# Kernel optimization log

Measured on AMD Instinct MI355X. Metric: run time of the kernel, lower is better.

Reference implementation:

```python
import jax, jax.numpy as jnp
import numpy as np

B, N, D_IN, D_OUT = 4, 2048, 1024, 1024


def setup_inputs() -> dict:
    key = jax.random.key(0)
    kx, kq, kk, kv = jax.random.split(key, 4)
    x = jax.random.normal(kx, (B, N, D_IN), dtype=jnp.float32)
    # torch Linear(d_in, d_out, bias=False): y = x @ W.T, W ~ U(-1/sqrt(d_in), 1/sqrt(d_in)).
    # Store as [d_in, d_out] so y = x @ W.
    bound = 1.0 / np.sqrt(D_IN)
    Wq = jax.random.uniform(kq, (D_IN, D_OUT), jnp.float32, -bound, bound)
    Wk = jax.random.uniform(kk, (D_IN, D_OUT), jnp.float32, -bound, bound)
    Wv = jax.random.uniform(kv, (D_IN, D_OUT), jnp.float32, -bound, bound)
    return {"x": x, "Wq": Wq, "Wk": Wk, "Wv": Wv}


def reference(x, Wq, Wk, Wv):
    # x: [B, N, d_in]
    q = jnp.einsum("bnd,de->bne", x, Wq)  # [B, N, d_out]
    k = jnp.einsum("bnd,de->bne", x, Wk)
    v = jnp.einsum("bnd,de->bne", x, Wv)
    n = x.shape[1]
    scores = jnp.einsum("bqe,bke->bqk", q, k)  # [B, N, N]
    causal = jnp.triu(jnp.ones((n, n), dtype=bool), k=1)  # True above diagonal -> masked
    scores = jnp.where(causal, -jnp.inf, scores)
    scale = 1.0 / jnp.sqrt(jnp.asarray(k.shape[-1], dtype=scores.dtype))
    weights = jax.nn.softmax(scores * scale, axis=-1)
    # dropout with drop_rate=0.0 is identity
    return jnp.einsum("bqk,bke->bqe", weights, v)  # [B, N, d_out]
```

## Files before the change

### kernel.cpp

```cpp
#include <hip/hip_runtime.h>

typedef float  f4v  __attribute__((ext_vector_type(4)));
typedef short  s8v  __attribute__((ext_vector_type(8)));

__device__ __forceinline__ ushort f2b(float f) {
    union { float f; unsigned int u; } v; v.f = f;
    unsigned int u = v.u;
    u += 0x7fffu + ((u >> 16) & 1u);
    return (ushort)(u >> 16);
}
__device__ __forceinline__ float b2f(ushort u) {
    union { unsigned int u; float f; } v; v.u = ((unsigned int)u) << 16;
    return v.f;
}

__device__ __forceinline__ void async16(const ushort* g, ushort* ldsp) {
    __builtin_amdgcn_global_load_lds(
        (const __attribute__((address_space(1))) unsigned int*)g,
        (__attribute__((address_space(3))) unsigned int*)ldsp, 16, 0, 0);
}

__global__ __launch_bounds__(256) void prep(const float* __restrict__ in,
                                            ushort* __restrict__ out,
                                            float* __restrict__ l,
                                            const float* __restrict__ w0,
                                            const float* __restrict__ w1,
                                            const float* __restrict__ w2,
                                            ushort* __restrict__ wt) {
    const int L = blockIdx.x, tid = threadIdx.x;
    if (L < 8192) {
        int i = L * 256 + tid;
        if (i < 8192) l[i] = 0.f;
        float4 f = ((const float4*)in)[i];
        ushort4 o;
        o.x = f2b(f.x); o.y = f2b(f.y); o.z = f2b(f.z); o.w = f2b(f.w);
        ((ushort4*)out)[i] = o;
        return;
    }
    __shared__ float tile[32][33];
    const int T = L - 8192;
    const int z = T >> 10, rem = T & 1023;
    const int bx = rem & 31, by = rem >> 5;
    const float* W = (z == 0) ? w0 : (z == 1 ? w1 : w2);
    ushort* O = wt + (size_t)z * (1024u * 1024u);
    int x0 = bx * 32, y0 = by * 32;
    int tx = tid & 31, ty = tid >> 5;
    for (int i = 0; i < 4; i++)
        tile[ty + i * 8][tx] = W[(size_t)(y0 + ty + i * 8) * 1024 + x0 + tx];
    __syncthreads();
    for (int i = 0; i < 4; i++)
        O[(size_t)(x0 + ty + i * 8) * 1024 + y0 + tx] = f2b(tile[tx][ty + i * 8]);
}


#define RD_A4(buf_)                                                                   \
    _Pragma("unroll") for (int mi = 0; mi < 4; mi++)                                  \
    _Pragma("unroll") for (int s = 0; s < 2; s++)                                     \
        af[mi][s] = *(const s8v*)&(buf_)[(wm + mi * 16 + l16) * 64 +                  \
                                         (((s * 4 + quad) ^ (l16 & 7)) * 8)];

#define RD_B2(buf_, NI0_)                                                             \
    _Pragma("unroll") for (int j = 0; j < 2; j++)                                     \
    _Pragma("unroll") for (int s = 0; s < 2; s++)                                     \
        bf[j][s] = *(const s8v*)&(buf_)[(wn + ((NI0_) + j) * 16 + l16) * 64 +         \
                                        (((s * 4 + quad) ^ (l16 & 7)) * 8)];

#define MFMA16(NI0_)                                                                  \
    _Pragma("unroll") for (int mi = 0; mi < 4; mi++)                                  \
    _Pragma("unroll") for (int j = 0; j < 2; j++)                                     \
    _Pragma("unroll") for (int s = 0; s < 2; s++)                                     \
        acc[mi][(NI0_) + j] = __builtin_amdgcn_mfma_f32_16x16x32_bf16(                \
            af[mi][s], bf[j][s], acc[mi][(NI0_) + j], 0, 0, 0);

#define RD_A4_TO(dst_, buf_)                                                          \
    _Pragma("unroll") for (int mi = 0; mi < 4; mi++)                                  \
    _Pragma("unroll") for (int s = 0; s < 2; s++)                                     \
        dst_[mi][s] = *(const s8v*)&(buf_)[(wm + mi * 16 + l16) * 64 +                \
                                           (((s * 4 + quad) ^ (l16 & 7)) * 8)];

#define RD_B2_TO(dst_, buf_, NI0_)                                                    \
    _Pragma("unroll") for (int j = 0; j < 2; j++)                                     \
    _Pragma("unroll") for (int s = 0; s < 2; s++)                                     \
        dst_[j][s] = *(const s8v*)&(buf_)[(wn + ((NI0_) + j) * 16 + l16) * 64 +       \
                                          (((s * 4 + quad) ^ (l16 & 7)) * 8)];

#define MFMA16F(af_, bf_, NI0_)                                                       \
    _Pragma("unroll") for (int mi = 0; mi < 4; mi++)                                  \
    _Pragma("unroll") for (int j = 0; j < 2; j++)                                     \
    _Pragma("unroll") for (int s = 0; s < 2; s++)                                     \
        acc[mi][(NI0_) + j] = __builtin_amdgcn_mfma_f32_16x16x32_bf16(                \
            af_[mi][s], bf_[j][s], acc[mi][(NI0_) + j], 0, 0, 0);

#define TILE3_NB(t_)                                                                  \
  {                                                                                   \
    const int kB = ((t_) + 1) * 64;                                                   \
    const int kA = ((t_) + 2) * 64;                                                   \
    s8v af[4][2], bf[2][2];                                                           \
    RD_A4(a0)                                                                         \
    RD_B2(b0, 0)                                                                      \
    if ((t_) < 15) {                                                                  \
        ISSUE_B(b1, kB, 0);                                                           \
        ISSUE_B(b1, kB, 1);                                                           \
        ISSUE_B(b1, kB, 2);                                                           \
    }                                                                                 \
    __builtin_amdgcn_s_setprio(1);                                                    \
    MFMA16(0)                                                                         \
    __builtin_amdgcn_s_setprio(0);                                                    \
    RD_B2(b0, 2)                                                                      \
    if ((t_) < 14) {                                                                  \
        ISSUE_A(a2, kA, 0);                                                           \
        ISSUE_A(a2, kA, 1);                                                           \
    }                                                                                 \
    __builtin_amdgcn_s_setprio(1);                                                    \
    MFMA16(2)                                                                         \
    __builtin_amdgcn_s_setprio(0);                                                    \
    RD_B2(b0, 4)                                                                      \
    if ((t_) < 14) {                                                                  \
        ISSUE_A(a2, kA, 2);                                                           \
        ISSUE_A(a2, kA, 3);                                                           \
    }                                                                                 \
    __builtin_amdgcn_s_setprio(1);                                                    \
    MFMA16(4)                                                                         \
    __builtin_amdgcn_s_setprio(0);                                                    \
    if ((t_) < 14)       asm volatile("s_waitcnt vmcnt(4)" ::: "memory");             \
    else if ((t_) == 14) asm volatile("s_waitcnt vmcnt(0)" ::: "memory");             \
    asm volatile("s_barrier" ::: "memory");                                           \
    ushort* ta = a0; a0 = a1; a1 = a2; a2 = ta;                                       \
    ushort* tb = b0; b0 = b1; b1 = tb;                                                \
  }

__global__ __launch_bounds__(512, 2) void gemm_qkv(const ushort* __restrict__ A,
                                                   const ushort* __restrict__ Wt,
                                                   ushort* __restrict__ q,
                                                   ushort* __restrict__ k,
                                                   ushort* __restrict__ vt) {
    constexpr int K = 1024;
    extern __shared__ ushort lds[];

    const int L = blockIdx.x;
    const int xcd = L & 7, idx = L >> 3;
    const int ci = xcd >> 1, cj = xcd & 1;
    const int mo = idx >> 3, no = idx & 7;
    const int m0 = (ci * 8 + mo) * 256;
    const int n0 = (cj * 8 + no) * 192;

    const int tid = threadIdx.x;
    const int w = tid >> 6, lane = tid & 63, quad = lane >> 4, l16 = lane & 15;
    const int wm = (w >> 1) * 64, wn = (w & 1) * 96;

    ushort* a0 = lds;
    ushort* a1 = lds + 16384;
    ushort* a2 = lds + 32768;
    ushort* b0 = lds + 49152;
    ushort* b1 = lds + 61440;

    const int lr = lane >> 3;
    const int lc8 = (lane & 7) ^ lr;
    const ushort* Ab = A  + (size_t)(m0 + w * 8 + lr) * K + lc8 * 8;
    const ushort* Bb = Wt + (size_t)(n0 + w * 8 + lr) * K + lc8 * 8;
    const int dW = w * 512;

#define ISSUE_A(buf_, kk_, a_) async16(Ab + (size_t)(a_) * 64 * K + (kk_), (buf_) + (a_) * 4096 + dW)
#define ISSUE_B(buf_, kk_, c_) async16(Bb + (size_t)(c_) * 64 * K + (kk_), (buf_) + (c_) * 4096 + dW)

    f4v acc[4][6];
    #pragma unroll
    for (int mi = 0; mi < 4; mi++)
        #pragma unroll
        for (int ni = 0; ni < 6; ni++) acc[mi][ni] = 0;

    #pragma unroll
    for (int a = 0; a < 4; a++) ISSUE_A(a0, 0, a);
    #pragma unroll
    for (int c = 0; c < 3; c++) ISSUE_B(b0, 0, c);
    #pragma unroll
    for (int a = 0; a < 4; a++) ISSUE_A(a1, 64, a);
    asm volatile("s_waitcnt vmcnt(4)" ::: "memory");
    asm volatile("s_barrier" ::: "memory");

    for (int t = 0; t < 16; ++t) TILE3_NB(t)

    #pragma unroll
    for (int mi = 0; mi < 4; mi++)
        #pragma unroll
        for (int ni = 0; ni < 6; ni++) {
            int row = m0 + wm + mi * 16 + quad * 4;
            int col = n0 + wn + ni * 16 + l16;
            int z = col >> 10, cz = col & 1023;
            f4v v = acc[mi][ni];
            if (z < 2) {
                ushort* C = (z == 0) ? q : k;
                #pragma unroll
                for (int rr = 0; rr < 4; rr++)
                    C[(size_t)(row + rr) * 1024 + cz] = f2b(v[rr]);
            } else {
                int b = row >> 11, tok = row & 2047;
                ushort4 pk;
                pk.x = f2b(v[0]); pk.y = f2b(v[1]); pk.z = f2b(v[2]); pk.w = f2b(v[3]);
                *(ushort4*)&vt[(size_t)b * (1024u * 2048u) + (size_t)cz * 2048 + tok] = pk;
            }
        }
#undef ISSUE_A
#undef ISSUE_B
}

__global__ __launch_bounds__(512, 2) void sgemm_qk(const ushort* __restrict__ Q,
                                                   const ushort* __restrict__ Km,
                                                   ushort* __restrict__ E,
                                                   float* __restrict__ l) {
    constexpr int K = 1024;
    extern __shared__ ushort lds[];

    const int L = blockIdx.x;
    const int xcd = L & 7, i = L >> 3;
    const int t = (xcd < 4) ? (xcd * 26 + i) : (104 + (xcd - 4) * 25 + i);
    const int b = t / 51;
    int tt = t - b * 51;
    int mt = 0;
    for (;; mt++) {
        int c = (4 * (mt + 1) + 2) / 3;
        if (tt < c) break;
        tt -= c;
    }
    const int nt = tt;
    const int m0 = mt * 256, n0 = nt * 192;
    const ushort* A  = Q  + (size_t)b * 2048 * 1024;
    const ushort* Bt = Km + (size_t)b * 2048 * 1024;
    ushort* Cb = E + (size_t)b * 2048 * 2048;
    float* lb = l + (size_t)b * 2048;

    const int tid = threadIdx.x;
    const int w = tid >> 6, lane = tid & 63, quad = lane >> 4, l16 = lane & 15;
    const int wm = (w >> 1) * 64, wn = (w & 1) * 96;

    ushort* a0 = lds;
    ushort* a1 = lds + 16384;
    ushort* a2 = lds + 32768;
    ushort* b0 = lds + 49152;
    ushort* b1 = lds + 61440;

    const int lr = lane >> 3;
    const int lc8 = (lane & 7) ^ lr;
    const ushort* Ab = A  + (size_t)(m0 + w * 8 + lr) * K + lc8 * 8;
    const ushort* Bb = Bt + (size_t)(n0 + w * 8 + lr) * K + lc8 * 8;
    const int dW = w * 512;

#define ISSUE_A(buf_, kk_, a_) async16(Ab + (size_t)(a_) * 64 * K + (kk_), (buf_) + (a_) * 4096 + dW)
#define ISSUE_B(buf_, kk_, c_) async16(Bb + (size_t)(c_) * 64 * K + (kk_), (buf_) + (c_) * 4096 + dW)

    f4v acc[4][6];
    #pragma unroll
    for (int mi = 0; mi < 4; mi++)
        #pragma unroll
        for (int ni = 0; ni < 6; ni++) acc[mi][ni] = 0;

    #pragma unroll
    for (int a = 0; a < 4; a++) ISSUE_A(a0, 0, a);
    #pragma unroll
    for (int c = 0; c < 3; c++) ISSUE_B(b0, 0, c);
    #pragma unroll
    for (int a = 0; a < 4; a++) ISSUE_A(a1, 64, a);
    asm volatile("s_waitcnt vmcnt(4)" ::: "memory");
    asm volatile("s_barrier" ::: "memory");

    for (int tk = 0; tk < 16; ++tk) TILE3_NB(tk)

    #pragma unroll
    for (int mi = 0; mi < 4; mi++) {
        float rs[4] = {0.f, 0.f, 0.f, 0.f};
        #pragma unroll
        for (int ni = 0; ni < 6; ni++) {
            const int colbase = n0 + wn + ni * 16;
            if (colbase >= 2048) continue;
            const int col = colbase + l16;
            f4v v = acc[mi][ni];
            #pragma unroll
            for (int rr = 0; rr < 4; rr++) {
                const int row = m0 + wm + mi * 16 + quad * 4 + rr;
                float e = (col <= row) ? __expf(v[rr] * 0.03125f) : 0.f;
                ushort eb = f2b(e);
                Cb[(size_t)row * 2048 + col] = eb;
                rs[rr] += b2f(eb);
            }
        }
        #pragma unroll
        for (int rr = 0; rr < 4; rr++) {
            float s = rs[rr];
            s += __shfl_xor(s, 1);
            s += __shfl_xor(s, 2);
            s += __shfl_xor(s, 4);
            s += __shfl_xor(s, 8);
            if (l16 == 0)
                atomicAdd(&lb[m0 + wm + mi * 16 + quad * 4 + rr], s);
        }
    }
#undef ISSUE_A
#undef ISSUE_B
}

__global__ __launch_bounds__(512, 2) void gemm_pv(const ushort* __restrict__ Em,
                                                  const ushort* __restrict__ Vt,
                                                  const float* __restrict__ l,
                                                  float* __restrict__ Out) {
    extern __shared__ ushort lds[];
    const int L = blockIdx.x;
    const int p = (L & 7) * 32 + (L >> 3);
    const int pair = p >> 5;
    const int inner = p & 31;
    const int b = inner >> 3;
    const int nt = inner & 7;
    const int n0 = nt * 128;
    const ushort* A  = Em + (size_t)b * 2048 * 2048;
    const ushort* Bt = Vt + (size_t)b * 1024 * 2048;
    const float* lb = l + (size_t)b * 2048;
    float* C = Out + (size_t)b * 2048 * 1024;

    const int tid = threadIdx.x;
    const int w = tid >> 6, lane = tid & 63, quad = lane >> 4, l16 = lane & 15;
    const int wm = (w >> 2) * 64, wn = (w & 3) * 32;

    const int lr = lane >> 3;
    const int lc8 = (lane & 7) ^ lr;
    const int dW = w * 512;

#define ISSUE_A(buf_, kk_, a_) async16(Ab + (size_t)(a_) * 64 * 2048 + (kk_), (buf_) + (a_) * 4096 + dW)
#define ISSUE_B(buf_, kk_, c_) async16(Bb + (size_t)(c_) * 64 * 2048 + (kk_), (buf_) + (c_) * 4096 + dW)

#define TILE1(t_, FCA_, FCB_, FNA_, FNB_)                                             \
  {                                                                                   \
    const int kk = ((t_) + 2) * 64;                                                   \
    if ((t_) < NT - 2) {                                                              \
        ISSUE_A(a2, kk, 0); ISSUE_A(a2, kk, 1);                                       \
        ISSUE_B(b2, kk, 0); ISSUE_B(b2, kk, 1);                                       \
        asm volatile("s_waitcnt vmcnt(4)" ::: "memory");                              \
    } else if ((t_) == NT - 2) {                                                      \
        asm volatile("s_waitcnt vmcnt(0)" ::: "memory");                              \
    }                                                                                 \
    asm volatile("s_barrier" ::: "memory");                                           \
    RD_A4_TO(FNA_, a1)                                                                \
    RD_B2_TO(FNB_, b1, 0)                                                             \
    __builtin_amdgcn_s_setprio(1);                                                    \
    MFMA16F(FCA_, FCB_, 0)                                                            \
    __builtin_amdgcn_s_setprio(0);                                                    \
    ushort* ta = a0; a0 = a1; a1 = a2; a2 = ta;                                       \
    ushort* tb = b0; b0 = b1; b1 = b2; b2 = tb;                                       \
  }

    #pragma unroll
    for (int half = 0; half < 2; ++half) {
        const int mt = half ? (15 - pair) : pair;
        const int m0 = mt * 128;
        const int NT = 2 * (mt + 1);

        ushort* a0 = lds;
        ushort* a1 = lds + 8192;
        ushort* a2 = lds + 16384;
        ushort* b0 = lds + 24576;
        ushort* b1 = lds + 32768;
        ushort* b2 = lds + 40960;

        const ushort* Ab = A  + (size_t)(m0 + w * 8 + lr) * 2048 + lc8 * 8;
        const ushort* Bb = Bt + (size_t)(n0 + w * 8 + lr) * 2048 + lc8 * 8;

        f4v acc[4][2];
        #pragma unroll
        for (int mi = 0; mi < 4; mi++)
            #pragma unroll
            for (int ni = 0; ni < 2; ni++) acc[mi][ni] = 0;

        asm volatile("s_barrier" ::: "memory");

        ISSUE_A(a0, 0, 0); ISSUE_A(a0, 0, 1);
        ISSUE_B(b0, 0, 0); ISSUE_B(b0, 0, 1);
        ISSUE_A(a1, 64, 0); ISSUE_A(a1, 64, 1);
        ISSUE_B(b1, 64, 0); ISSUE_B(b1, 64, 1);
        asm volatile("s_waitcnt vmcnt(4)" ::: "memory");
        asm volatile("s_barrier" ::: "memory");

        s8v afX[4][2], bfX[2][2], afY[4][2], bfY[2][2];
        RD_A4_TO(afX, a0)
        RD_B2_TO(bfX, b0, 0)
        for (int tk = 0; tk < NT; tk += 2) {
            TILE1(tk,     afX, bfX, afY, bfY)
            TILE1(tk + 1, afY, bfY, afX, bfX)
        }

        #pragma unroll
        for (int mi = 0; mi < 4; mi++) {
            const int row = m0 + wm + mi * 16 + quad * 4;
            float inv[4];
            #pragma unroll
            for (int rr = 0; rr < 4; rr++) inv[rr] = 1.f / lb[row + rr];
            #pragma unroll
            for (int ni = 0; ni < 2; ni++) {
                const int col = n0 + wn + ni * 16 + l16;
                f4v v = acc[mi][ni];
                #pragma unroll
                for (int rr = 0; rr < 4; rr++)
                    C[(size_t)(row + rr) * 1024 + col] = v[rr] * inv[rr];
            }
        }
    }
#undef TILE1
#undef ISSUE_A
#undef ISSUE_B
}

extern "C" void kernel_launch(void* const* d_in, const int* in_sizes, int n_in,
                              void* d_out, int out_size, void* d_ws, size_t ws_size,
                              hipStream_t stream) {
    const float* x  = (const float*)d_in[0];
    const float* Wq = (const float*)d_in[1];
    const float* Wk = (const float*)d_in[2];
    const float* Wv = (const float*)d_in[3];
    float* out = (float*)d_out;

    static bool init = false;
    if (!init) {
        hipFuncSetAttribute(reinterpret_cast<const void*>(gemm_qkv),
                            hipFuncAttributeMaxDynamicSharedMemorySize, 147456);
        hipFuncSetAttribute(reinterpret_cast<const void*>(sgemm_qk),
                            hipFuncAttributeMaxDynamicSharedMemorySize, 147456);
        hipFuncSetAttribute(reinterpret_cast<const void*>(gemm_pv),
                            hipFuncAttributeMaxDynamicSharedMemorySize, 98304);
        init = true;
    }

    char* ws = (char*)d_ws;
    const size_t MiB = 1u << 20;
    ushort* xb = (ushort*)(ws);
    ushort* wt = (ushort*)(ws + 16 * MiB);
    ushort* q  = (ushort*)(ws + 22 * MiB);
    ushort* k  = (ushort*)(ws + 38 * MiB);
    ushort* vt = (ushort*)(ws + 54 * MiB);
    ushort* E  = (ushort*)(ws + 70 * MiB);
    float*  l  = (float*)(ws + 102 * MiB);

    prep<<<8192 + 3072, 256, 0, stream>>>(x, xb, l, Wq, Wk, Wv, wt);

    gemm_qkv<<<512, 512, 147456, stream>>>(xb, wt, q, k, vt);
    sgemm_qk<<<204, 512, 147456, stream>>>(q, k, E, l);
    gemm_pv<<<256, 512, 98304, stream>>>(E, vt, l, out);
}
```

Before: 208.8 us.

## Halve wave count in QKV and QK GEMMs, doubling per-wave M tile

The QKV projection and QK^T score GEMMs now launch 4 waves (256 threads) per block instead of 8. Each wave computes a 128x96 sub-tile (8x6 MFMA accumulators) instead of 64x96, and the async global-to-LDS load assignment is remapped so each wave loads contiguous 8-row groups. The goal is more register-level reuse of the B fragments and fewer LDS reads per MFMA. The cost is doubled accumulator registers, which may hurt occupancy or cause spills, and fewer waves to hide latency (launch bounds 256,1).

```diff
diff --git a/kernel.cpp b/kernel.cpp
--- a/kernel.cpp
+++ b/kernel.cpp
@@ -53,8 +53,8 @@
 }
 
 
-#define RD_A4(buf_)                                                                   \
-    _Pragma("unroll") for (int mi = 0; mi < 4; mi++)                                  \
+#define RD_A8(buf_)                                                                   \
+    _Pragma("unroll") for (int mi = 0; mi < 8; mi++)                                  \
     _Pragma("unroll") for (int s = 0; s < 2; s++)                                     \
         af[mi][s] = *(const s8v*)&(buf_)[(wm + mi * 16 + l16) * 64 +                  \
                                          (((s * 4 + quad) ^ (l16 & 7)) * 8)];
@@ -65,8 +65,8 @@
         bf[j][s] = *(const s8v*)&(buf_)[(wn + ((NI0_) + j) * 16 + l16) * 64 +         \
                                         (((s * 4 + quad) ^ (l16 & 7)) * 8)];
 
-#define MFMA16(NI0_)                                                                  \
-    _Pragma("unroll") for (int mi = 0; mi < 4; mi++)                                  \
+#define MFMA32(NI0_)                                                                  \
+    _Pragma("unroll") for (int mi = 0; mi < 8; mi++)                                  \
     _Pragma("unroll") for (int j = 0; j < 2; j++)                                     \
     _Pragma("unroll") for (int s = 0; s < 2; s++)                                     \
         acc[mi][(NI0_) + j] = __builtin_amdgcn_mfma_f32_16x16x32_bf16(                \
@@ -91,45 +91,44 @@
         acc[mi][(NI0_) + j] = __builtin_amdgcn_mfma_f32_16x16x32_bf16(                \
             af_[mi][s], bf_[j][s], acc[mi][(NI0_) + j], 0, 0, 0);
 
-#define TILE3_NB(t_)                                                                  \
+#define TILE3_NB4(t_)                                                                 \
   {                                                                                   \
     const int kB = ((t_) + 1) * 64;                                                   \
     const int kA = ((t_) + 2) * 64;                                                   \
-    s8v af[4][2], bf[2][2];                                                           \
-    RD_A4(a0)                                                                         \
+    s8v af[8][2], bf[2][2];                                                           \
+    RD_A8(a0)                                                                         \
     RD_B2(b0, 0)                                                                      \
     if ((t_) < 15) {                                                                  \
-        ISSUE_B(b1, kB, 0);                                                           \
-        ISSUE_B(b1, kB, 1);                                                           \
-        ISSUE_B(b1, kB, 2);                                                           \
+        ISSUE_B(b1, kB, 0); ISSUE_B(b1, kB, 1); ISSUE_B(b1, kB, 2);                   \
+        ISSUE_B(b1, kB, 3); ISSUE_B(b1, kB, 4); ISSUE_B(b1, kB, 5);                   \
     }                                                                                 \
     __builtin_amdgcn_s_setprio(1);                                                    \
-    MFMA16(0)                                                                         \
+    MFMA32(0)                                                                         \
     __builtin_amdgcn_s_setprio(0);                                                    \
     RD_B2(b0, 2)                                                                      \
     if ((t_) < 14) {                                                                  \
-        ISSUE_A(a2, kA, 0);                                                           \
-        ISSUE_A(a2, kA, 1);                                                           \
+        ISSUE_A(a2, kA, 0); ISSUE_A(a2, kA, 1);                                       \
+        ISSUE_A(a2, kA, 2); ISSUE_A(a2, kA, 3);                                       \
     }                                                                                 \
     __builtin_amdgcn_s_setprio(1);                                                    \
-    MFMA16(2)                                                                         \
+    MFMA32(2)                                                                         \
     __builtin_amdgcn_s_setprio(0);                                                    \
     RD_B2(b0, 4)                                                                      \
     if ((t_) < 14) {                                                                  \
-        ISSUE_A(a2, kA, 2);                                                           \
-        ISSUE_A(a2, kA, 3);                                                           \
+        ISSUE_A(a2, kA, 4); ISSUE_A(a2, kA, 5);                                       \
+        ISSUE_A(a2, kA, 6); ISSUE_A(a2, kA, 7);                                       \
     }                                                                                 \
     __builtin_amdgcn_s_setprio(1);                                                    \
-    MFMA16(4)                                                                         \
+    MFMA32(4)                                                                         \
     __builtin_amdgcn_s_setprio(0);                                                    \
-    if ((t_) < 14)       asm volatile("s_waitcnt vmcnt(4)" ::: "memory");             \
+    if ((t_) < 14)       asm volatile("s_waitcnt vmcnt(8)" ::: "memory");             \
     else if ((t_) == 14) asm volatile("s_waitcnt vmcnt(0)" ::: "memory");             \
     asm volatile("s_barrier" ::: "memory");                                           \
     ushort* ta = a0; a0 = a1; a1 = a2; a2 = ta;                                       \
     ushort* tb = b0; b0 = b1; b1 = tb;                                                \
   }
 
-__global__ __launch_bounds__(512, 2) void gemm_qkv(const ushort* __restrict__ A,
+__global__ __launch_bounds__(256, 1) void gemm_qkv(const ushort* __restrict__ A,
                                                    const ushort* __restrict__ Wt,
                                                    ushort* __restrict__ q,
                                                    ushort* __restrict__ k,
@@ -146,7 +145,7 @@
 
     const int tid = threadIdx.x;
     const int w = tid >> 6, lane = tid & 63, quad = lane >> 4, l16 = lane & 15;
-    const int wm = (w >> 1) * 64, wn = (w & 1) * 96;
+    const int wm = (w >> 1) * 128, wn = (w & 1) * 96;
 
     ushort* a0 = lds;
     ushort* a1 = lds + 16384;
@@ -156,32 +155,33 @@
 
     const int lr = lane >> 3;
     const int lc8 = (lane & 7) ^ lr;
-    const ushort* Ab = A  + (size_t)(m0 + w * 8 + lr) * K + lc8 * 8;
-    const ushort* Bb = Wt + (size_t)(n0 + w * 8 + lr) * K + lc8 * 8;
-    const int dW = w * 512;
-
-#define ISSUE_A(buf_, kk_, a_) async16(Ab + (size_t)(a_) * 64 * K + (kk_), (buf_) + (a_) * 4096 + dW)
-#define ISSUE_B(buf_, kk_, c_) async16(Bb + (size_t)(c_) * 64 * K + (kk_), (buf_) + (c_) * 4096 + dW)
-
-    f4v acc[4][6];
-    #pragma unroll
-    for (int mi = 0; mi < 4; mi++)
+    const ushort* Ab = A  + (size_t)(m0 + w * 64 + lr) * K + lc8 * 8;
+    const ushort* Bb = Wt + (size_t)(n0 + w * 48 + lr) * K + lc8 * 8;
+    const int dWA = w * 4096;
+    const int dWB = w * 3072;
+
+#define ISSUE_A(buf_, kk_, j_) async16(Ab + (size_t)(j_) * 8 * K + (kk_), (buf_) + (j_) * 512 + dWA)
+#define ISSUE_B(buf_, kk_, j_) async16(Bb + (size_t)(j_) * 8 * K + (kk_), (buf_) + (j_) * 512 + dWB)
+
+    f4v acc[8][6];
+    #pragma unroll
+    for (int mi = 0; mi < 8; mi++)
         #pragma unroll
         for (int ni = 0; ni < 6; ni++) acc[mi][ni] = 0;
 
     #pragma unroll
-    for (int a = 0; a < 4; a++) ISSUE_A(a0, 0, a);
-    #pragma unroll
-    for (int c = 0; c < 3; c++) ISSUE_B(b0, 0, c);
-    #pragma unroll
-    for (int a = 0; a < 4; a++) ISSUE_A(a1, 64, a);
-    asm volatile("s_waitcnt vmcnt(4)" ::: "memory");
+    for (int j = 0; j < 8; j++) ISSUE_A(a0, 0, j);
+    #pragma unroll
+    for (int j = 0; j < 6; j++) ISSUE_B(b0, 0, j);
+    #pragma unroll
+    for (int j = 0; j < 8; j++) ISSUE_A(a1, 64, j);
+    asm volatile("s_waitcnt vmcnt(8)" ::: "memory");
     asm volatile("s_barrier" ::: "memory");
 
-    for (int t = 0; t < 16; ++t) TILE3_NB(t)
-
-    #pragma unroll
-    for (int mi = 0; mi < 4; mi++)
+    for (int t = 0; t < 16; ++t) TILE3_NB4(t)
+
+    #pragma unroll
+    for (int mi = 0; mi < 8; mi++)
         #pragma unroll
         for (int ni = 0; ni < 6; ni++) {
             int row = m0 + wm + mi * 16 + quad * 4;
@@ -204,7 +204,7 @@
 #undef ISSUE_B
 }
 
-__global__ __launch_bounds__(512, 2) void sgemm_qk(const ushort* __restrict__ Q,
+__global__ __launch_bounds__(256, 1) void sgemm_qk(const ushort* __restrict__ Q,
                                                    const ushort* __restrict__ Km,
                                                    ushort* __restrict__ E,
                                                    float* __restrict__ l) {
@@ -231,7 +231,7 @@
 
     const int tid = threadIdx.x;
     const int w = tid >> 6, lane = tid & 63, quad = lane >> 4, l16 = lane & 15;
-    const int wm = (w >> 1) * 64, wn = (w & 1) * 96;
+    const int wm = (w >> 1) * 128, wn = (w & 1) * 96;
 
     ushort* a0 = lds;
     ushort* a1 = lds + 16384;
@@ -241,32 +241,33 @@
 
     const int lr = lane >> 3;
     const int lc8 = (lane & 7) ^ lr;
-    const ushort* Ab = A  + (size_t)(m0 + w * 8 + lr) * K + lc8 * 8;
-    const ushort* Bb = Bt + (size_t)(n0 + w * 8 + lr) * K + lc8 * 8;
-    const int dW = w * 512;
-
-#define ISSUE_A(buf_, kk_, a_) async16(Ab + (size_t)(a_) * 64 * K + (kk_), (buf_) + (a_) * 4096 + dW)
-#define ISSUE_B(buf_, kk_, c_) async16(Bb + (size_t)(c_) * 64 * K + (kk_), (buf_) + (c_) * 4096 + dW)
-
-    f4v acc[4][6];
-    #pragma unroll
-    for (int mi = 0; mi < 4; mi++)
+    const ushort* Ab = A  + (size_t)(m0 + w * 64 + lr) * K + lc8 * 8;
+    const ushort* Bb = Bt + (size_t)(n0 + w * 48 + lr) * K + lc8 * 8;
+    const int dWA = w * 4096;
+    const int dWB = w * 3072;
+
+#define ISSUE_A(buf_, kk_, j_) async16(Ab + (size_t)(j_) * 8 * K + (kk_), (buf_) + (j_) * 512 + dWA)
+#define ISSUE_B(buf_, kk_, j_) async16(Bb + (size_t)(j_) * 8 * K + (kk_), (buf_) + (j_) * 512 + dWB)
+
+    f4v acc[8][6];
+    #pragma unroll
+    for (int mi = 0; mi < 8; mi++)
         #pragma unroll
         for (int ni = 0; ni < 6; ni++) acc[mi][ni] = 0;
 
     #pragma unroll
-    for (int a = 0; a < 4; a++) ISSUE_A(a0, 0, a);
-    #pragma unroll
-    for (int c = 0; c < 3; c++) ISSUE_B(b0, 0, c);
-    #pragma unroll
-    for (int a = 0; a < 4; a++) ISSUE_A(a1, 64, a);
-    asm volatile("s_waitcnt vmcnt(4)" ::: "memory");
+    for (int j = 0; j < 8; j++) ISSUE_A(a0, 0, j);
+    #pragma unroll
+    for (int j = 0; j < 6; j++) ISSUE_B(b0, 0, j);
+    #pragma unroll
+    for (int j = 0; j < 8; j++) ISSUE_A(a1, 64, j);
+    asm volatile("s_waitcnt vmcnt(8)" ::: "memory");
     asm volatile("s_barrier" ::: "memory");
 
-    for (int tk = 0; tk < 16; ++tk) TILE3_NB(tk)
-
-    #pragma unroll
-    for (int mi = 0; mi < 4; mi++) {
+    for (int tk = 0; tk < 16; ++tk) TILE3_NB4(tk)
+
+    #pragma unroll
+    for (int mi = 0; mi < 8; mi++) {
         float rs[4] = {0.f, 0.f, 0.f, 0.f};
         #pragma unroll
         for (int ni = 0; ni < 6; ni++) {
@@ -438,7 +439,7 @@
 
     prep<<<8192 + 3072, 256, 0, stream>>>(x, xb, l, Wq, Wk, Wv, wt);
 
-    gemm_qkv<<<512, 512, 147456, stream>>>(xb, wt, q, k, vt);
-    sgemm_qk<<<204, 512, 147456, stream>>>(q, k, E, l);
+    gemm_qkv<<<512, 256, 147456, stream>>>(xb, wt, q, k, vt);
+    sgemm_qk<<<204, 256, 147456, stream>>>(q, k, E, l);
     gemm_pv<<<256, 512, 98304, stream>>>(E, vt, l, out);
 }
```

Measured after the change: 216.1 us. 1.03x slower.

## Retile QKV projection GEMM to 256x256 tiles with quadrant-interleaved pipeline

Applied to the files above, without the earlier changes.

The fused QKV projection GEMM moves from 256x192 tiles (512 blocks) to 256x256 tiles (384 blocks). The main loop now splits each K-step into four quadrant MFMA phases that are interleaved with the async global-to-LDS loads of the next stage. A two-buffer LDS scheme replaces the old triple-A/double-B buffers, and setprio is raised around the MFMA bursts. The aim is more arithmetic per loaded byte and better overlap of loads with compute, at the cost of fewer blocks, a larger accumulator array, and many more barriers per iteration.

```diff
diff --git a/kernel.cpp b/kernel.cpp
--- a/kernel.cpp
+++ b/kernel.cpp
@@ -140,54 +140,121 @@
     const int L = blockIdx.x;
     const int xcd = L & 7, idx = L >> 3;
     const int ci = xcd >> 1, cj = xcd & 1;
-    const int mo = idx >> 3, no = idx & 7;
+    const int mo = idx / 6, no = idx - mo * 6;
     const int m0 = (ci * 8 + mo) * 256;
-    const int n0 = (cj * 8 + no) * 192;
+    const int n0 = (cj * 6 + no) * 256;
 
     const int tid = threadIdx.x;
     const int w = tid >> 6, lane = tid & 63, quad = lane >> 4, l16 = lane & 15;
-    const int wm = (w >> 1) * 64, wn = (w & 1) * 96;
-
-    ushort* a0 = lds;
-    ushort* a1 = lds + 16384;
-    ushort* a2 = lds + 32768;
-    ushort* b0 = lds + 49152;
-    ushort* b1 = lds + 61440;
+    const int wrm = (w >> 2) * 64;
+    const int wrn = (w & 3) * 32;
+
+    ushort* cur = lds;
+    ushort* oth = lds + 32768;
 
     const int lr = lane >> 3;
     const int lc8 = (lane & 7) ^ lr;
-    const ushort* Ab = A  + (size_t)(m0 + w * 8 + lr) * K + lc8 * 8;
-    const ushort* Bb = Wt + (size_t)(n0 + w * 8 + lr) * K + lc8 * 8;
-    const int dW = w * 512;
-
-#define ISSUE_A(buf_, kk_, a_) async16(Ab + (size_t)(a_) * 64 * K + (kk_), (buf_) + (a_) * 4096 + dW)
-#define ISSUE_B(buf_, kk_, c_) async16(Bb + (size_t)(c_) * 64 * K + (kk_), (buf_) + (c_) * 4096 + dW)
-
-    f4v acc[4][6];
-    #pragma unroll
-    for (int mi = 0; mi < 4; mi++)
-        #pragma unroll
-        for (int ni = 0; ni < 6; ni++) acc[mi][ni] = 0;
-
-    #pragma unroll
-    for (int a = 0; a < 4; a++) ISSUE_A(a0, 0, a);
-    #pragma unroll
-    for (int c = 0; c < 3; c++) ISSUE_B(b0, 0, c);
-    #pragma unroll
-    for (int a = 0; a < 4; a++) ISSUE_A(a1, 64, a);
-    asm volatile("s_waitcnt vmcnt(4)" ::: "memory");
-    asm volatile("s_barrier" ::: "memory");
-
-    for (int t = 0; t < 16; ++t) TILE3_NB(t)
-
-    #pragma unroll
-    for (int mi = 0; mi < 4; mi++)
-        #pragma unroll
-        for (int ni = 0; ni < 6; ni++) {
-            int row = m0 + wm + mi * 16 + quad * 4;
-            int col = n0 + wn + ni * 16 + l16;
+    const ushort* ABASE = A  + (size_t)(m0 + w * 16 + lr) * K + lc8 * 8;
+    const ushort* BBASE = Wt + (size_t)(n0 + w * 16 + lr) * K + lc8 * 8;
+    const int dW = w * 1024;
+
+#define STAGE_A(buf_, kk_, h_)                                                        \
+    do {                                                                              \
+        async16(ABASE + (size_t)(h_) * 128 * K + (kk_), (buf_) + (h_) * 8192 + dW);   \
+        async16(ABASE + (size_t)(h_) * 128 * K + 8 * K + (kk_),                       \
+                (buf_) + (h_) * 8192 + dW + 512);                                     \
+    } while (0)
+#define STAGE_B(buf_, kk_, h_)                                                        \
+    do {                                                                              \
+        async16(BBASE + (size_t)(h_) * 128 * K + (kk_),                               \
+                (buf_) + 16384 + (h_) * 8192 + dW);                                   \
+        async16(BBASE + (size_t)(h_) * 128 * K + 8 * K + (kk_),                       \
+                (buf_) + 16384 + (h_) * 8192 + dW + 512);                             \
+    } while (0)
+
+#define RD_AQ(qm_)                                                                    \
+    _Pragma("unroll") for (int mi = 0; mi < 4; mi++)                                  \
+    _Pragma("unroll") for (int s = 0; s < 2; s++)                                     \
+        af[mi][s] = *(const s8v*)&cur[(qm_) * 8192 +                                  \
+            (wrm + mi * 16 + l16) * 64 + (((s * 4 + quad) ^ (l16 & 7)) * 8)];
+
+#define RD_BQ(qn_)                                                                    \
+    _Pragma("unroll") for (int nj = 0; nj < 2; nj++)                                  \
+    _Pragma("unroll") for (int s = 0; s < 2; s++)                                     \
+        bf[nj][s] = *(const s8v*)&cur[16384 + (qn_) * 8192 +                          \
+            (wrn + nj * 16 + l16) * 64 + (((s * 4 + quad) ^ (l16 & 7)) * 8)];
+
+#define MFMAQ(QM_, QN_)                                                               \
+    _Pragma("unroll") for (int mi = 0; mi < 4; mi++)                                  \
+    _Pragma("unroll") for (int nj = 0; nj < 2; nj++)                                  \
+    _Pragma("unroll") for (int s = 0; s < 2; s++)                                     \
+        acc[(QM_) * 4 + mi][(QN_) * 2 + nj] = __builtin_amdgcn_mfma_f32_16x16x32_bf16(\
+            af[mi][s], bf[nj][s], acc[(QM_) * 4 + mi][(QN_) * 2 + nj], 0, 0, 0);
+
+#define BAR asm volatile("s_barrier" ::: "memory")
+
+    f4v acc[8][4];
+    #pragma unroll
+    for (int mi = 0; mi < 8; mi++)
+        #pragma unroll
+        for (int ni = 0; ni < 4; ni++) acc[mi][ni] = 0;
+
+    STAGE_A(cur, 0, 0); STAGE_B(cur, 0, 0); STAGE_B(cur, 0, 1); STAGE_A(cur, 0, 1);
+    STAGE_A(oth, 64, 0); STAGE_B(oth, 64, 1); STAGE_A(oth, 64, 1);
+    asm volatile("s_waitcnt vmcnt(6)" ::: "memory");
+    BAR;
+
+    for (int t = 0; t < 16; ++t) {
+        const int kB = (t + 1) * 64;
+        const int kA = (t + 2) * 64;
+        s8v af[4][2], bf[2][2];
+
+        RD_AQ(0)
+        RD_BQ(0)
+        if (t < 15) STAGE_B(oth, kB, 0);
+        BAR;
+        __builtin_amdgcn_s_setprio(1);
+        MFMAQ(0, 0)
+        __builtin_amdgcn_s_setprio(0);
+        BAR;
+
+        RD_BQ(1)
+        if (t < 14) STAGE_A(cur, kA, 0);
+        BAR;
+        __builtin_amdgcn_s_setprio(1);
+        MFMAQ(0, 1)
+        __builtin_amdgcn_s_setprio(0);
+        BAR;
+
+        RD_AQ(1)
+        if (t < 14) STAGE_B(cur, kA, 1);
+        BAR;
+        __builtin_amdgcn_s_setprio(1);
+        MFMAQ(1, 1)
+        __builtin_amdgcn_s_setprio(0);
+        BAR;
+
+        RD_BQ(0)
+        if (t < 14) STAGE_A(cur, kA, 1);
+        if (t < 14)       asm volatile("s_waitcnt vmcnt(6)" ::: "memory");
+        else if (t == 14) asm volatile("s_waitcnt vmcnt(0)" ::: "memory");
+        BAR;
+        __builtin_amdgcn_s_setprio(1);
+        MFMAQ(1, 0)
+        __builtin_amdgcn_s_setprio(0);
+        BAR;
+
+        ushort* tswp = cur; cur = oth; oth = tswp;
+    }
+
+    #pragma unroll
+    for (int MI = 0; MI < 8; MI++)
+        #pragma unroll
+        for (int NJ = 0; NJ < 4; NJ++) {
+            int row = m0 + (MI >> 2) * 128 + wrm + (MI & 3) * 16 + quad * 4;
+            int col = n0 + (NJ >> 1) * 128 + wrn + (NJ & 1) * 16 + l16;
             int z = col >> 10, cz = col & 1023;
-            f4v v = acc[mi][ni];
+            f4v v = acc[MI][NJ];
             if (z < 2) {
                 ushort* C = (z == 0) ? q : k;
                 #pragma unroll
@@ -200,8 +267,12 @@
                 *(ushort4*)&vt[(size_t)b * (1024u * 2048u) + (size_t)cz * 2048 + tok] = pk;
             }
         }
-#undef ISSUE_A
-#undef ISSUE_B
+#undef STAGE_A
+#undef STAGE_B
+#undef RD_AQ
+#undef RD_BQ
+#undef MFMAQ
+#undef BAR
 }
 
 __global__ __launch_bounds__(512, 2) void sgemm_qk(const ushort* __restrict__ Q,
@@ -418,7 +489,7 @@
     static bool init = false;
     if (!init) {
         hipFuncSetAttribute(reinterpret_cast<const void*>(gemm_qkv),
-                            hipFuncAttributeMaxDynamicSharedMemorySize, 147456);
+                            hipFuncAttributeMaxDynamicSharedMemorySize, 131072);
         hipFuncSetAttribute(reinterpret_cast<const void*>(sgemm_qk),
                             hipFuncAttributeMaxDynamicSharedMemorySize, 147456);
         hipFuncSetAttribute(reinterpret_cast<const void*>(gemm_pv),
@@ -438,7 +509,7 @@
 
     prep<<<8192 + 3072, 256, 0, stream>>>(x, xb, l, Wq, Wk, Wv, wt);
 
-    gemm_qkv<<<512, 512, 147456, stream>>>(xb, wt, q, k, vt);
+    gemm_qkv<<<384, 512, 131072, stream>>>(xb, wt, q, k, vt);
     sgemm_qk<<<204, 512, 147456, stream>>>(q, k, E, l);
     gemm_pv<<<256, 512, 98304, stream>>>(E, vt, l, out);
 }
```

Measured after the change: 219.0 us. 4.9% more time.
